# Performance work log

Hardware: AMD Instinct MI355X
Metric: run time of the kernel (lower is better)

The kernel has to match this reference:

```python
import jax, jax.numpy as jnp
import numpy as np

B, C, W, H = 16, 512, 64, 64
D = 16  # linear out features


def setup_inputs() -> dict:
    key = jax.random.key(0)
    k1, k2, k3, k4, k5 = jax.random.split(key, 5)
    x = jax.random.normal(k1, (B, C, W, H), dtype=jnp.float32)
    # nn.LazyLinear(16) with in_features = W*H
    Wq = jax.random.normal(k2, (D, W * H), dtype=jnp.float32) * 0.02
    bq = jnp.zeros((D,), dtype=jnp.float32)
    Wk = jax.random.normal(k3, (D, W * H), dtype=jnp.float32) * 0.02
    bk = jnp.zeros((D,), dtype=jnp.float32)
    return {"x": x, "Wq": Wq, "bq": bq, "Wk": Wk, "bk": bk}


def reference(x, Wq, bq, Wk, bk):
    b, c, w, h = x.shape
    xf = x.reshape(b, c, w * h)                      # [B, C, W*H]
    q = jnp.einsum('bcs,ds->bcd', xf, Wq) + bq       # [B, C, 16]
    k = jnp.einsum('bcs,ds->bcd', xf, Wk) + bk       # [B, C, 16]
    kq = jnp.einsum('bcd,bed->bce', q, k)            # [B, C, C]
    # torch nn.Softmax2d applies softmax over dim -3; for the 3D tensor
    # [B, C, C] that is the batch axis (axis 0) -- faithful reproduction.
    A = jax.nn.softmax(kq, axis=0)                   # [B, C, C]
    # Per-sample 1x1 conv with weight[o, i] = A[b, i, o] (note the transpose
    # from the permute([3,2,1,0]) in the torch code).
    out = jnp.einsum('bio,biwh->bowh', A, x)         # [B, C, W, H]
    return out
```

## Files before the change

### kernel.cpp

```cpp
#include <hip/hip_runtime.h>
#include <hip/hip_bf16.h>
#include <stdint.h>

typedef __attribute__((ext_vector_type(8))) short short8;
typedef __attribute__((ext_vector_type(4))) float floatx4;

#define B_ 16
#define C_ 512
#define S_ 4096
#define D_ 16

__device__ __forceinline__ unsigned short f2bf(float f) {
    union { float f; unsigned int i; } v;
    v.f = f;
    unsigned int u = v.i;
    return (unsigned short)((u + 0x7FFFu + ((u >> 16) & 1u)) >> 16);
}
__device__ __forceinline__ unsigned int pack2bf(float lo, float hi) {
    __hip_bfloat162 h = __float22bfloat162_rn(make_float2(lo, hi));
    union { __hip_bfloat162 h; unsigned int u; } v;
    v.h = h;
    return v.u;
}
__device__ __forceinline__ short8 cvt8p(float4 a, float4 b) {
    union { unsigned int u[4]; short8 s; } r;
    r.u[0] = pack2bf(a.x, a.y);
    r.u[1] = pack2bf(a.z, a.w);
    r.u[2] = pack2bf(b.x, b.y);
    r.u[3] = pack2bf(b.z, b.w);
    return r.s;
}

__device__ __forceinline__ void gl16(const void* g, void* l) {
    __builtin_amdgcn_global_load_lds(
        (const __attribute__((address_space(1))) unsigned int*)g,
        (__attribute__((address_space(3))) unsigned int*)l, 16, 0, 0);
}

template <int NS>
__global__ __launch_bounds__(256) void qk_kernel(
    const float* __restrict__ x,
    const float* __restrict__ Wq,
    const float* __restrict__ bq,
    const float* __restrict__ Wk,
    const float* __restrict__ bk,
    float* __restrict__ qkp)
{
    int lane = threadIdx.x & 63;
    int w    = threadIdx.x >> 6;
    int gw   = blockIdx.x * 4 + w;
    int row_tile = gw / NS;
    int ks       = gw % NS;
    int m  = lane & 15;
    int q8 = lane >> 4;
    int k0 = ks * (S_ / NS);

    const float* ax = x  + (size_t)(row_tile * 16 + m) * S_ + k0 + q8 * 8;
    const float* aq = Wq + (size_t)m * S_ + k0 + q8 * 8;
    const float* ak = Wk + (size_t)m * S_ + k0 + q8 * 8;

    floatx4 accq = {0.f, 0.f, 0.f, 0.f};
    floatx4 acck = {0.f, 0.f, 0.f, 0.f};
#pragma unroll 4
    for (int it = 0; it < S_ / NS / 32; ++it) {
        float4 xa = *(const float4*)(ax + it * 32);
        float4 xb2 = *(const float4*)(ax + it * 32 + 4);
        float4 qa = *(const float4*)(aq + it * 32);
        float4 qb = *(const float4*)(aq + it * 32 + 4);
        float4 ka = *(const float4*)(ak + it * 32);
        float4 kb2 = *(const float4*)(ak + it * 32 + 4);
        short8 a   = cvt8p(xa, xb2);
        short8 bq8 = cvt8p(qa, qb);
        short8 bk8 = cvt8p(ka, kb2);
        accq = __builtin_amdgcn_mfma_f32_16x16x32_bf16(a, bq8, accq, 0, 0, 0);
        acck = __builtin_amdgcn_mfma_f32_16x16x32_bf16(a, bk8, acck, 0, 0, 0);
    }
    float biasq = (ks == 0) ? bq[m] : 0.f;
    float biask = (ks == 0) ? bk[m] : 0.f;
    float* outp = qkp + (size_t)ks * 8192 * 32;
#pragma unroll
    for (int r = 0; r < 4; ++r) {
        int row = row_tile * 16 + q8 * 4 + r;
        outp[(size_t)row * 32 + m]      = accq[r] + biasq;
        outp[(size_t)row * 32 + 16 + m] = acck[r] + biask;
    }
}

template <int NS>
__global__ __launch_bounds__(256) void reduce_kernel(
    const float* __restrict__ qkp, float* __restrict__ qred)
{
    int g = blockIdx.x * 256 + threadIdx.x;
    const float4* p = (const float4*)qkp + g;
    float4 r = p[0];
#pragma unroll
    for (int k = 1; k < NS; ++k) {
        float4 v = p[(size_t)k * 65536];
        r.x += v.x; r.y += v.y; r.z += v.z; r.w += v.w;
    }
    ((float4*)qred)[g] = r;
}

__global__ __launch_bounds__(512) void softmax_kernel(
    const float* __restrict__ qred,
    unsigned short* __restrict__ Abf)
{
    __shared__ float lq[B_][32][17];
    __shared__ float lk[B_][16][17];
    int i0 = blockIdx.x * 32;
    int o0 = blockIdx.y * 16;
    int tid = threadIdx.x;

    {
        int d = tid & 15, il = tid >> 4;
#pragma unroll
        for (int b = 0; b < 16; ++b)
            lq[b][il][d] = qred[(size_t)(b * C_ + i0 + il) * 32 + d];
    }
    if (tid < 256) {
        int d = tid & 15, ol = tid >> 4;
#pragma unroll
        for (int b = 0; b < 16; ++b)
            lk[b][ol][d] = qred[(size_t)(b * C_ + o0 + ol) * 32 + 16 + d];
    }
    __syncthreads();

    int i = tid & 31;
    int o = tid >> 5;
    float v[16];
#pragma unroll
    for (int b = 0; b < 16; ++b) {
        float s = 0.f;
#pragma unroll
        for (int d = 0; d < 16; ++d) s += lq[b][i][d] * lk[b][o][d];
        v[b] = s;
    }
    float mx = v[0];
#pragma unroll
    for (int b = 1; b < 16; ++b) mx = fmaxf(mx, v[b]);
    float sum = 0.f;
#pragma unroll
    for (int b = 0; b < 16; ++b) { v[b] = __expf(v[b] - mx); sum += v[b]; }
    float inv = 1.0f / sum;
#pragma unroll
    for (int b = 0; b < 16; ++b)
        Abf[(size_t)(b * C_ + o0 + o) * C_ + i0 + i] = f2bf(v[b] * inv);
}

#define XP 36

__global__ __launch_bounds__(256) void av_kernel(
    const unsigned short* __restrict__ Abf,
    const float* __restrict__ x,
    float* __restrict__ out)
{
    __shared__ unsigned int At[128 * 32];
    __shared__ unsigned int Xt[128 * XP];
    int b  = blockIdx.z;
    int o0 = blockIdx.y * 128;
    int s0 = blockIdx.x * 128;
    int tid  = threadIdx.x;
    int lane = tid & 63;
    int w    = tid >> 6;
    int wm = (w >> 1) * 64;
    int wn = (w & 1) * 64;
    int fm = lane & 15;
    int q8 = lane >> 4;

    floatx4 acc[4][4];
#pragma unroll
    for (int a = 0; a < 4; ++a)
#pragma unroll
        for (int c = 0; c < 4; ++c) acc[a][c] = (floatx4){0.f, 0.f, 0.f, 0.f};

    const unsigned short* Ab = Abf + (size_t)b * C_ * C_;
    const float* xb = x + (size_t)b * C_ * S_;

    int arow_l = (lane >> 3);
    int acol   = (lane & 7) * 8;

    int xc  = tid >> 3;
    int xip = tid & 7;

    for (int kb = 0; kb < 8; ++kb) {
        int i0 = kb * 64;
#pragma unroll
        for (int q = 0; q < 4; ++q) {
            const unsigned short* gp =
                Ab + (size_t)(o0 + w * 32 + q * 8 + arow_l) * C_ + i0 + acol;
            unsigned int* lp = At + (w * 32 + q * 8) * 32;
            gl16(gp, lp);
        }
#pragma unroll
        for (int r = 0; r < 4; ++r) {
            int ip = r * 8 + xip;
            const float* x0 = xb + (size_t)(i0 + 2 * ip) * S_ + s0 + xc * 4;
            float4 va = *(const float4*)x0;
            float4 vb = *(const float4*)(x0 + S_);
            unsigned int* dst = &Xt[(xc * 4) * XP + ip];
            dst[0 * XP] = pack2bf(va.x, vb.x);
            dst[1 * XP] = pack2bf(va.y, vb.y);
            dst[2 * XP] = pack2bf(va.z, vb.z);
            dst[3 * XP] = pack2bf(va.w, vb.w);
        }
        __syncthreads();

#pragma unroll
        for (int kc = 0; kc < 2; ++kc) {
            short8 af[4], bfr[4];
#pragma unroll
            for (int t = 0; t < 4; ++t)
                af[t] = *(const short8*)(&At[(wm + t * 16 + fm) * 32 + kc * 16 + q8 * 4]);
#pragma unroll
            for (int t = 0; t < 4; ++t)
                bfr[t] = *(const short8*)(&Xt[(wn + t * 16 + fm) * XP + kc * 16 + q8 * 4]);
#pragma unroll
            for (int a = 0; a < 4; ++a)
#pragma unroll
                for (int c = 0; c < 4; ++c)
                    acc[a][c] = __builtin_amdgcn_mfma_f32_16x16x32_bf16(af[a], bfr[c], acc[a][c], 0, 0, 0);
        }
        __syncthreads();
    }

    float* ob = out + (size_t)b * C_ * S_;
#pragma unroll
    for (int a = 0; a < 4; ++a) {
        int orow = o0 + wm + a * 16 + q8 * 4;
#pragma unroll
        for (int c = 0; c < 4; ++c) {
            int sc = s0 + wn + c * 16 + fm;
#pragma unroll
            for (int r = 0; r < 4; ++r)
                ob[(size_t)(orow + r) * S_ + sc] = acc[a][c][r];
        }
    }
}

extern "C" void kernel_launch(void* const* d_in, const int* in_sizes, int n_in,
                              void* d_out, int out_size, void* d_ws, size_t ws_size,
                              hipStream_t stream) {
    const float* x  = (const float*)d_in[0];
    const float* Wq = (const float*)d_in[1];
    const float* bq = (const float*)d_in[2];
    const float* Wk = (const float*)d_in[3];
    const float* bk = (const float*)d_in[4];
    float* out = (float*)d_out;

    if (ws_size >= (size_t)17 * 1024 * 1024) {
        float* qkp = (float*)d_ws;
        float* qred = (float*)((char*)d_ws + (size_t)8 * 1024 * 1024);
        unsigned short* Abf =
            (unsigned short*)((char*)d_ws + (size_t)9 * 1024 * 1024);
        qk_kernel<8><<<1024, 256, 0, stream>>>(x, Wq, bq, Wk, bk, qkp);
        reduce_kernel<8><<<256, 256, 0, stream>>>(qkp, qred);
        softmax_kernel<<<dim3(16, 32), 512, 0, stream>>>(qred, Abf);
        av_kernel<<<dim3(32, 4, 16), 256, 0, stream>>>(Abf, x, out);
    } else {
        float* qkp = (float*)d_ws;
        float* qred = (float*)((char*)d_ws + (size_t)4 * 1024 * 1024);
        unsigned short* Abf =
            (unsigned short*)((char*)d_ws + (size_t)5 * 1024 * 1024);
        qk_kernel<4><<<512, 256, 0, stream>>>(x, Wq, bq, Wk, bk, qkp);
        reduce_kernel<4><<<256, 256, 0, stream>>>(qkp, qred);
        softmax_kernel<<<dim3(16, 32), 512, 0, stream>>>(qred, Abf);
        av_kernel<<<dim3(32, 4, 16), 256, 0, stream>>>(Abf, x, out);
    }
}
```

Measured before the change: 327.2 us.

## Stage qk inputs through LDS with prefetch and swizzle av A-tile layout

The qk projection kernel now has each block cooperatively load 64 rows of x plus the Wq/Wk slices into padded shared memory, with a register prefetch of the next chunk. The weight loads are shared across four waves instead of being re-fetched by every wave, and x is read in coalesced rows. The av kernel also XOR-swizzles the column placement of the A tile in LDS to cut bank conflicts on fragment reads. The cost is extra block barriers and LDS traffic in the qk kernel.

```diff
diff --git a/kernel.cpp b/kernel.cpp
--- a/kernel.cpp
+++ b/kernel.cpp
@@ -36,6 +36,8 @@
         (const __attribute__((address_space(1))) unsigned int*)g,
         (__attribute__((address_space(3))) unsigned int*)l, 16, 0, 0);
 }
+
+#define QP 68
 
 template <int NS>
 __global__ __launch_bounds__(256) void qk_kernel(
@@ -46,43 +48,76 @@
     const float* __restrict__ bk,
     float* __restrict__ qkp)
 {
-    int lane = threadIdx.x & 63;
-    int w    = threadIdx.x >> 6;
-    int gw   = blockIdx.x * 4 + w;
-    int row_tile = gw / NS;
-    int ks       = gw % NS;
-    int m  = lane & 15;
+    constexpr int KCH = S_ / NS;
+    constexpr int NK  = KCH / 64;
+    __shared__ float Xs[64 * QP];
+    __shared__ float Ws[32 * QP];
+    int tid  = threadIdx.x;
+    int lane = tid & 63;
+    int w    = tid >> 6;
+    int rt = blockIdx.x & 127;
+    int ks = blockIdx.x >> 7;
+    int r0 = rt * 64;
+    int k0 = ks * KCH;
+    int fm = lane & 15;
     int q8 = lane >> 4;
-    int k0 = ks * (S_ / NS);
-
-    const float* ax = x  + (size_t)(row_tile * 16 + m) * S_ + k0 + q8 * 8;
-    const float* aq = Wq + (size_t)m * S_ + k0 + q8 * 8;
-    const float* ak = Wk + (size_t)m * S_ + k0 + q8 * 8;
+
+    int su = tid >> 4;
+    int sv = tid & 15;
+
+    const float* xbase  = x  + (size_t)(r0 + su) * S_ + k0 + sv * 4;
+    const float* wqbase = Wq + (size_t)su * S_ + k0 + sv * 4;
+    const float* wkbase = Wk + (size_t)su * S_ + k0 + sv * 4;
 
     floatx4 accq = {0.f, 0.f, 0.f, 0.f};
     floatx4 acck = {0.f, 0.f, 0.f, 0.f};
-#pragma unroll 4
-    for (int it = 0; it < S_ / NS / 32; ++it) {
-        float4 xa = *(const float4*)(ax + it * 32);
-        float4 xb2 = *(const float4*)(ax + it * 32 + 4);
-        float4 qa = *(const float4*)(aq + it * 32);
-        float4 qb = *(const float4*)(aq + it * 32 + 4);
-        float4 ka = *(const float4*)(ak + it * 32);
-        float4 kb2 = *(const float4*)(ak + it * 32 + 4);
-        short8 a   = cvt8p(xa, xb2);
-        short8 bq8 = cvt8p(qa, qb);
-        short8 bk8 = cvt8p(ka, kb2);
-        accq = __builtin_amdgcn_mfma_f32_16x16x32_bf16(a, bq8, accq, 0, 0, 0);
-        acck = __builtin_amdgcn_mfma_f32_16x16x32_bf16(a, bk8, acck, 0, 0, 0);
-    }
-    float biasq = (ks == 0) ? bq[m] : 0.f;
-    float biask = (ks == 0) ? bk[m] : 0.f;
+
+    float4 xv[4], wv[2];
+#pragma unroll
+    for (int i = 0; i < 4; ++i)
+        xv[i] = *(const float4*)(xbase + (size_t)16 * i * S_);
+    wv[0] = *(const float4*)(wqbase);
+    wv[1] = *(const float4*)(wkbase);
+
+    for (int kk = 0; kk < NK; ++kk) {
+#pragma unroll
+        for (int i = 0; i < 4; ++i)
+            *(float4*)(&Xs[(16 * i + su) * QP + sv * 4]) = xv[i];
+        *(float4*)(&Ws[su * QP + sv * 4])        = wv[0];
+        *(float4*)(&Ws[(16 + su) * QP + sv * 4]) = wv[1];
+        __syncthreads();
+
+        if (kk + 1 < NK) {
+            int off = (kk + 1) * 64;
+#pragma unroll
+            for (int i = 0; i < 4; ++i)
+                xv[i] = *(const float4*)(xbase + (size_t)16 * i * S_ + off);
+            wv[0] = *(const float4*)(wqbase + off);
+            wv[1] = *(const float4*)(wkbase + off);
+        }
+
+#pragma unroll
+        for (int kc = 0; kc < 2; ++kc) {
+            const float* xr  = &Xs[(w * 16 + fm) * QP + kc * 32 + q8 * 8];
+            const float* wqr = &Ws[fm * QP + kc * 32 + q8 * 8];
+            const float* wkr = &Ws[(16 + fm) * QP + kc * 32 + q8 * 8];
+            short8 a   = cvt8p(*(const float4*)xr,  *(const float4*)(xr + 4));
+            short8 bq8 = cvt8p(*(const float4*)wqr, *(const float4*)(wqr + 4));
+            short8 bk8 = cvt8p(*(const float4*)wkr, *(const float4*)(wkr + 4));
+            accq = __builtin_amdgcn_mfma_f32_16x16x32_bf16(a, bq8, accq, 0, 0, 0);
+            acck = __builtin_amdgcn_mfma_f32_16x16x32_bf16(a, bk8, acck, 0, 0, 0);
+        }
+        __syncthreads();
+    }
+
+    float biasq = (ks == 0) ? bq[fm] : 0.f;
+    float biask = (ks == 0) ? bk[fm] : 0.f;
     float* outp = qkp + (size_t)ks * 8192 * 32;
 #pragma unroll
     for (int r = 0; r < 4; ++r) {
-        int row = row_tile * 16 + q8 * 4 + r;
-        outp[(size_t)row * 32 + m]      = accq[r] + biasq;
-        outp[(size_t)row * 32 + 16 + m] = acck[r] + biask;
+        int row = r0 + w * 16 + q8 * 4 + r;
+        outp[(size_t)row * 32 + fm]      = accq[r] + biasq;
+        outp[(size_t)row * 32 + 16 + fm] = acck[r] + biask;
     }
 }
 
@@ -176,8 +211,8 @@
     const unsigned short* Ab = Abf + (size_t)b * C_ * C_;
     const float* xb = x + (size_t)b * C_ * S_;
 
-    int arow_l = (lane >> 3);
-    int acol   = (lane & 7) * 8;
+    int arow_l = lane >> 3;
+    int acol   = ((lane & 7) ^ (arow_l & 7)) * 8;
 
     int xc  = tid >> 3;
     int xip = tid & 7;
@@ -210,7 +245,8 @@
             short8 af[4], bfr[4];
 #pragma unroll
             for (int t = 0; t < 4; ++t)
-                af[t] = *(const short8*)(&At[(wm + t * 16 + fm) * 32 + kc * 16 + q8 * 4]);
+                af[t] = *(const short8*)(&At[(wm + t * 16 + fm) * 32 +
+                                             (((kc * 4 + q8) ^ (fm & 7)) << 2)]);
 #pragma unroll
             for (int t = 0; t < 4; ++t)
                 bfr[t] = *(const short8*)(&Xt[(wn + t * 16 + fm) * XP + kc * 16 + q8 * 4]);
@@ -252,7 +288,7 @@
         float* qred = (float*)((char*)d_ws + (size_t)8 * 1024 * 1024);
         unsigned short* Abf =
             (unsigned short*)((char*)d_ws + (size_t)9 * 1024 * 1024);
-        qk_kernel<8><<<1024, 256, 0, stream>>>(x, Wq, bq, Wk, bk, qkp);
+        qk_kernel<8><<<128 * 8, 256, 0, stream>>>(x, Wq, bq, Wk, bk, qkp);
         reduce_kernel<8><<<256, 256, 0, stream>>>(qkp, qred);
         softmax_kernel<<<dim3(16, 32), 512, 0, stream>>>(qred, Abf);
         av_kernel<<<dim3(32, 4, 16), 256, 0, stream>>>(Abf, x, out);
@@ -261,7 +297,7 @@
         float* qred = (float*)((char*)d_ws + (size_t)4 * 1024 * 1024);
         unsigned short* Abf =
             (unsigned short*)((char*)d_ws + (size_t)5 * 1024 * 1024);
-        qk_kernel<4><<<512, 256, 0, stream>>>(x, Wq, bq, Wk, bk, qkp);
+        qk_kernel<4><<<128 * 4, 256, 0, stream>>>(x, Wq, bq, Wk, bk, qkp);
         reduce_kernel<4><<<256, 256, 0, stream>>>(qkp, qred);
         softmax_kernel<<<dim3(16, 32), 512, 0, stream>>>(qred, Abf);
         av_kernel<<<dim3(32, 4, 16), 256, 0, stream>>>(Abf, x, out);
```

Result: slower. 381.5 us (+16.6%).
